# Kernel tuning notes

Hardware: AMD Instinct MI355X
Metric: run time of the kernel (lower is better)

The kernel has to match this reference:

```python
import jax, jax.numpy as jnp
import numpy as np

# xLSTM '80k' config: 4 blocks (mLSTM at 0,2,3; sLSTM at 1)
B, S, F = 128, 256, 10      # batch, seq (= context_length = forecast_horizon), features
E, NH = 40, 8               # d_model, heads
DH = E // NH                # 5,  sLSTM per-head dim
I = 128                     # mLSTM inner dim = round64(2*E)
QKB = 4; NQK = I // QKB     # q/k/v block-diagonal proj: 32 blocks of 4
MDH = I // NH               # 16, mLSTM per-head dim
FFD = 64                    # gated FFN dim = round64(1.3*E)
K = 4                       # causal conv kernel
NMB = 3                     # number of mLSTM blocks


def layer_norm(x, w, eps=1e-5):
    mu = x.mean(-1, keepdims=True)
    return (x - mu) * jax.lax.rsqrt(x.var(-1, keepdims=True) + eps) * w


def multihead_norm(x, w, nh, eps=1e-5):
    # per-head group norm over D//nh channels, weight only
    b, s, d = x.shape
    xh = x.reshape(b, s, nh, d // nh)
    xh = (xh - xh.mean(-1, keepdims=True)) * jax.lax.rsqrt(xh.var(-1, keepdims=True) + eps)
    return xh.reshape(b, s, d) * w


def causal_conv(x, w, b):
    # depthwise causal conv1d, kernel K; x: (B,S,C), w: (C,K)
    xt = x.transpose(0, 2, 1)
    y = jax.lax.conv_general_dilated(xt, w[:, None, :], (1,), [(K - 1, 0)],
                                     feature_group_count=x.shape[-1],
                                     dimension_numbers=('NCH', 'OIH', 'NCH'))
    return (y + b[None, :, None]).transpose(0, 2, 1)


def headwise(x, w):
    # block-diagonal linear (LinearHeadwiseExpand, no bias): w (nb, bo, bi)
    nb, bo, bi = w.shape
    xh = x.reshape(*x.shape[:-1], nb, bi)
    return jnp.einsum('bsni,noi->bsno', xh, w).reshape(*x.shape[:-1], nb * bo)


def pos_encoding():
    pos = jnp.arange(S, dtype=jnp.float32)[:, None]
    div = jnp.exp(jnp.arange(0, E, 2, dtype=jnp.float32) * (-np.log(10000.0) / E))
    pe = jnp.zeros((S, E), jnp.float32)
    pe = pe.at[:, 0::2].set(jnp.sin(pos * div))
    pe = pe.at[:, 1::2].set(jnp.cos(pos * div))
    return pe


def mlstm_layer(x, up_w, conv_w, conv_b, q_w, k_w, v_w, ig_w, ig_b, fg_w, fg_b, mhn_w, skip, down_w):
    x_m, z = jnp.split(x @ up_w.T, 2, axis=-1)                 # each (B,S,I)
    x_c = jax.nn.silu(causal_conv(x_m, conv_w, conv_b))
    q, k, v = headwise(x_c, q_w), headwise(x_c, k_w), headwise(x_m, v_w)
    gin = jnp.concatenate([q, k, v], axis=-1)                   # (B,S,3I)
    ip = (gin @ ig_w.T + ig_b).transpose(0, 2, 1)               # (B,NH,S)
    fp = (gin @ fg_w.T + fg_b).transpose(0, 2, 1)
    heads = lambda t: t.reshape(B, S, NH, MDH).transpose(0, 2, 1, 3)
    qh, kh, vh = heads(q), heads(k), heads(v)
    # stabilized parallel mLSTM (parallel_stabilized_simple)
    Fc = jnp.cumsum(jax.nn.log_sigmoid(fp), axis=-1)
    log_fg = Fc[..., :, None] - Fc[..., None, :]                # (B,NH,S,S)
    mask = jnp.tril(jnp.ones((S, S), bool))
    log_D = jnp.where(mask, log_fg, -jnp.inf) + ip[..., None, :]
    mD = jnp.max(log_D, axis=-1, keepdims=True)
    D = jnp.exp(log_D - mD)
    qk = jnp.einsum('bhsd,bhtd->bhst', qh, kh) * (MDH ** -0.5)
    C = qk * D
    nrm = jnp.maximum(jnp.abs(C.sum(-1, keepdims=True)), jnp.exp(-mD))
    h = jnp.einsum('bhst,bhtd->bhsd', C / (nrm + 1e-6), vh)
    h = multihead_norm(h.transpose(0, 2, 1, 3).reshape(B, S, I), mhn_w, NH)
    return ((h + skip * x_c) * jax.nn.silu(z)) @ down_w.T


def slstm_layer(x, conv_w, conv_b, wi, wf, wz, wo, R, bias, mhn_w):
    x_c = jax.nn.silu(causal_conv(x, conv_w, conv_b))
    g = lambda inp, w: headwise(inp, w).reshape(B, S, NH, DH)
    # i,f from conv path; z,o from raw input (order i,f,z,o)
    gx = jnp.stack([g(x_c, wi), g(x_c, wf), g(x, wz), g(x, wo)], axis=3)  # (B,S,NH,4,DH)
    gx = gx.transpose(1, 0, 2, 3, 4)                                      # (S,B,NH,4,DH)

    def step(carry, g_t):
        h, c, n, m = carry
        raw = g_t + jnp.einsum('bhd,hgde->bhge', h, R) + bias
        i_r, f_r, z_r, o_r = raw[:, :, 0], raw[:, :, 1], raw[:, :, 2], raw[:, :, 3]
        logfplusm = m + jax.nn.log_sigmoid(f_r)
        m_new = jnp.maximum(i_r, logfplusm)
        ig, fg = jnp.exp(i_r - m_new), jnp.exp(logfplusm - m_new)
        c_new = fg * c + ig * jnp.tanh(z_r)
        n_new = fg * n + ig
        h_new = jax.nn.sigmoid(o_r) * c_new / n_new
        return (h_new, c_new, n_new, m_new), h_new

    z0 = jnp.zeros((B, NH, DH), jnp.float32)
    _, hs = jax.lax.scan(step, (z0, z0, z0, z0), gx)
    return multihead_norm(hs.transpose(1, 0, 2, 3).reshape(B, S, E), mhn_w, NH)


def _forward(x, in_proj_w, in_proj_b, m_ln_w, m_up_w, m_conv_w, m_conv_b, m_q_w, m_k_w, m_v_w,
             m_ig_w, m_ig_b, m_fg_w, m_fg_b, m_mhn_w, m_skip, m_down_w,
             s_ln1_w, s_conv_w, s_conv_b, s_wi, s_wf, s_wz, s_wo, s_R, s_b, s_mhn_w,
             s_ln2_w, s_ff_up_w, s_ff_down_w, post_ln_w, out_w, out_b):
    h = x @ in_proj_w.T + in_proj_b + pos_encoding()
    mb = lambda h, j: h + mlstm_layer(layer_norm(h, m_ln_w[j]), m_up_w[j], m_conv_w[j], m_conv_b[j],
                                      m_q_w[j], m_k_w[j], m_v_w[j], m_ig_w[j], m_ig_b[j],
                                      m_fg_w[j], m_fg_b[j], m_mhn_w[j], m_skip[j], m_down_w[j])
    h = mb(h, 0)                       # block 0: mLSTM
    # block 1: sLSTM + gated FFN (pre-LN residual)
    h = h + slstm_layer(layer_norm(h, s_ln1_w), s_conv_w, s_conv_b, s_wi, s_wf, s_wz, s_wo, s_R, s_b, s_mhn_w)
    gpre, up = jnp.split(layer_norm(h, s_ln2_w) @ s_ff_up_w.T, 2, axis=-1)
    h = h + (jax.nn.gelu(gpre, approximate=False) * up) @ s_ff_down_w.T
    h = mb(h, 1)                       # block 2: mLSTM
    h = mb(h, 2)                       # block 3: mLSTM
    return layer_norm(h, post_ln_w) @ out_w.T + out_b


def setup_inputs():
    ks = iter(jax.random.split(jax.random.key(0), 64))
    rn = lambda shape, fan: jax.random.normal(next(ks), shape, jnp.float32) * (fan ** -0.5)
    d = {}
    d['x'] = jax.random.normal(next(ks), (B, S, F), jnp.float32)
    d['in_proj_w'] = rn((E, F), F); d['in_proj_b'] = jnp.zeros((E,), jnp.float32)
    d['m_ln_w'] = jnp.ones((NMB, E), jnp.float32)
    d['m_up_w'] = rn((NMB, 2 * I, E), E)
    d['m_conv_w'] = rn((NMB, I, K), K); d['m_conv_b'] = jnp.zeros((NMB, I), jnp.float32)
    d['m_q_w'] = rn((NMB, NQK, QKB, QKB), QKB)
    d['m_k_w'] = rn((NMB, NQK, QKB, QKB), QKB)
    d['m_v_w'] = rn((NMB, NQK, QKB, QKB), QKB)
    d['m_ig_w'] = rn((NMB, NH, 3 * I), 3 * I); d['m_ig_b'] = jnp.zeros((NMB, NH), jnp.float32)
    d['m_fg_w'] = rn((NMB, NH, 3 * I), 3 * I); d['m_fg_b'] = 3.0 * jnp.ones((NMB, NH), jnp.float32)
    d['m_mhn_w'] = jnp.ones((NMB, I), jnp.float32); d['m_skip'] = jnp.ones((NMB, I), jnp.float32)
    d['m_down_w'] = rn((NMB, E, I), I)
    d['s_ln1_w'] = jnp.ones((E,), jnp.float32)
    d['s_conv_w'] = rn((E, K), K); d['s_conv_b'] = jnp.zeros((E,), jnp.float32)
    d['s_wi'] = rn((NH, DH, DH), DH); d['s_wf'] = rn((NH, DH, DH), DH)
    d['s_wz'] = rn((NH, DH, DH), DH); d['s_wo'] = rn((NH, DH, DH), DH)
    d['s_R'] = rn((NH, 4, DH, DH), DH); d['s_b'] = jnp.zeros((NH, 4, DH), jnp.float32)
    d['s_mhn_w'] = jnp.ones((E,), jnp.float32); d['s_ln2_w'] = jnp.ones((E,), jnp.float32)
    d['s_ff_up_w'] = rn((2 * FFD, E), E); d['s_ff_down_w'] = rn((E, FFD), FFD)
    d['post_ln_w'] = jnp.ones((E,), jnp.float32)
    d['out_w'] = rn((1, E), E); d['out_b'] = jnp.zeros((1,), jnp.float32)
    return d


def reference(x, in_proj_w, in_proj_b, m_ln_w, m_up_w, m_conv_w, m_conv_b, m_q_w, m_k_w, m_v_w,
              m_ig_w, m_ig_b, m_fg_w, m_fg_b, m_mhn_w, m_skip, m_down_w,
              s_ln1_w, s_conv_w, s_conv_b, s_wi, s_wf, s_wz, s_wo, s_R, s_b, s_mhn_w,
              s_ln2_w, s_ff_up_w, s_ff_down_w, post_ln_w, out_w, out_b):
    return _forward(x, in_proj_w, in_proj_b, m_ln_w, m_up_w, m_conv_w, m_conv_b, m_q_w, m_k_w, m_v_w,
                    m_ig_w, m_ig_b, m_fg_w, m_fg_b, m_mhn_w, m_skip, m_down_w,
                    s_ln1_w, s_conv_w, s_conv_b, s_wi, s_wf, s_wz, s_wo, s_R, s_b, s_mhn_w,
                    s_ln2_w, s_ff_up_w, s_ff_down_w, post_ln_w, out_w, out_b)
```

## Files before the change

kernel.cpp:

```cpp
#include <hip/hip_runtime.h>
#include <math.h>

constexpr int cB = 128, cS = 256, cF = 10, cE = 40, cNH = 8, cDH = 5;
constexpr int cI = 128, cMDH = 16, cK = 4;

typedef __attribute__((ext_vector_type(8))) short short8v;
typedef __attribute__((ext_vector_type(4))) float f32x4;

#define BC8(v, l) __uint_as_float(__builtin_amdgcn_ds_swizzle(__float_as_uint(v), ((l) << 5) | 0x18))

__device__ __forceinline__ short f2bf(float f) {
    unsigned u = __float_as_uint(f);
    u += 0x7FFF + ((u >> 16) & 1);
    return (short)(u >> 16);
}

__global__ __launch_bounds__(256) void init_k(const float* __restrict__ x, const float* __restrict__ w,
                                              const float* __restrict__ b, float* __restrict__ h) {
    int idx = blockIdx.x * 256 + threadIdx.x;
    int e = idx % cE; int bs = idx / cE; int s = bs % cS;
    float acc = b[e];
    const float* xr = x + (size_t)bs * cF;
#pragma unroll
    for (int f = 0; f < cF; ++f) acc += xr[f] * w[e * cF + f];
    int i2 = e >> 1;
    float div = expf(-(float)(2 * i2) * (logf(10000.f) / 40.0f));
    float arg = (float)s * div;
    acc += (e & 1) ? cosf(arg) : sinf(arg);
    h[idx] = acc;
}

__global__ __launch_bounds__(256) void ln_up_k(const float* __restrict__ h, const float* __restrict__ lnw,
                                               const float* __restrict__ upw, float* __restrict__ xmz) {
    __shared__ float lnr[16][cE];
    __shared__ float wT[cE * 257];
    int row0 = blockIdx.x * 16;
    int tid = threadIdx.x;
    for (int j = tid; j < 2560; j += 256) {
        float4 v = ((const float4*)upw)[j];
        int o = j / 10, kq = (j - o * 10) * 4;
        wT[(kq + 0) * 257 + o] = v.x;
        wT[(kq + 1) * 257 + o] = v.y;
        wT[(kq + 2) * 257 + o] = v.z;
        wT[(kq + 3) * 257 + o] = v.w;
    }
    if (tid < 16) {
        const float* r = h + (size_t)(row0 + tid) * cE;
        float mu = 0.f;
        for (int k = 0; k < cE; ++k) mu += r[k];
        mu *= (1.f / cE);
        float va = 0.f;
        for (int k = 0; k < cE; ++k) { float d = r[k] - mu; va += d * d; }
        va *= (1.f / cE);
        float rs = rsqrtf(va + 1e-5f);
        for (int k = 0; k < cE; ++k) lnr[tid][k] = (r[k] - mu) * rs * lnw[k];
    }
    __syncthreads();
    int o = tid;
    float acc[16];
#pragma unroll
    for (int r = 0; r < 16; ++r) acc[r] = 0.f;
    for (int k = 0; k < cE; ++k) {
        float wv = wT[k * 257 + o];
#pragma unroll
        for (int r = 0; r < 16; ++r) acc[r] = fmaf(lnr[r][k], wv, acc[r]);
    }
#pragma unroll
    for (int r = 0; r < 16; ++r) xmz[(size_t)(row0 + r) * 256 + o] = acc[r];
}

template <int C>
__global__ __launch_bounds__(256) void conv_silu_k(const float* __restrict__ in, int instride,
                                                   const float* __restrict__ w, const float* __restrict__ bias,
                                                   float* __restrict__ out) {
    int idx = blockIdx.x * 256 + threadIdx.x;
    int c = idx % C; int bs = idx / C; int s = bs % cS;
    float acc = bias[c];
#pragma unroll
    for (int j = 0; j < cK; ++j) {
        int sj = s - 3 + j;
        if (sj >= 0) acc += in[(size_t)(bs + j - 3) * instride + c] * w[c * cK + j];
    }
    float sg = 1.f / (1.f + __expf(-acc));
    out[idx] = acc * sg;
}

__global__ __launch_bounds__(256) void qkv_k(const float* __restrict__ xc, const float* __restrict__ xmz,
                                             const float* __restrict__ qw, const float* __restrict__ kw,
                                             const float* __restrict__ vw,
                                             float* __restrict__ qb, float* __restrict__ kb, float* __restrict__ vb) {
    int idx = blockIdx.x * 256 + threadIdx.x;
    int c = idx & 127; int bs = idx >> 7;
    int n = c >> 2, o = c & 3;
    const float* xcr = xc + (size_t)bs * cI + n * 4;
    const float* xmr = xmz + (size_t)bs * 256 + n * 4;
    const float* qwp = qw + n * 16 + o * 4;
    const float* kwp = kw + n * 16 + o * 4;
    const float* vwp = vw + n * 16 + o * 4;
    float aq = 0, ak = 0, av = 0;
#pragma unroll
    for (int i = 0; i < 4; ++i) { float a = xcr[i], m = xmr[i]; aq += a * qwp[i]; ak += a * kwp[i]; av += m * vwp[i]; }
    qb[idx] = aq; kb[idx] = ak; vb[idx] = av;
}

__global__ __launch_bounds__(256, 2) void gates_k(const float* __restrict__ qb, const float* __restrict__ kb,
                                                  const float* __restrict__ vb, const float* __restrict__ igw,
                                                  const float* __restrict__ igb, const float* __restrict__ fgw,
                                                  const float* __restrict__ fgb,
                                                  float* __restrict__ ipb, float* __restrict__ fpb) {
    __shared__ float g[32 * 388];
    __shared__ float w[16 * 388];
    int row0 = blockIdx.x * 32;
    int tid = threadIdx.x;

    for (int i = tid; i < 16 * 96; i += 256) {
        int r = i / 96, c4 = i - r * 96;
        const float* src = (r < 8) ? (igw + r * 384) : (fgw + (r - 8) * 384);
        *(float4*)&w[r * 388 + c4 * 4] = ((const float4*)src)[c4];
    }
    for (int i = tid; i < 32 * 96; i += 256) {
        int r = i / 96, c4 = i - r * 96;
        size_t gr = (size_t)(row0 + r) * cI;
        const float4* src = (c4 < 32) ? (const float4*)(qb + gr) + c4
                          : (c4 < 64) ? (const float4*)(kb + gr) + (c4 - 32)
                                      : (const float4*)(vb + gr) + (c4 - 64);
        *(float4*)&g[r * 388 + c4 * 4] = *src;
    }
    __syncthreads();

    int rp = tid >> 3;
    int hp = tid & 7;
    int o0 = 2 * hp, o1 = o0 + 1;

    const float4* gp = (const float4*)(g + rp * 388);
    const float4* w0p = (const float4*)(w + o0 * 388);
    const float4* w1p = (const float4*)(w + o1 * 388);

    float a0e = 0.f, a0o = 0.f, a1e = 0.f, a1o = 0.f;
#pragma unroll 2
    for (int c4 = 0; c4 < 96; c4 += 2) {
        float4 gv0 = gp[c4], gv1 = gp[c4 + 1];
        float4 wa0 = w0p[c4], wa1 = w0p[c4 + 1];
        float4 wb0 = w1p[c4], wb1 = w1p[c4 + 1];
        a0e = fmaf(gv0.x, wa0.x, a0e); a0e = fmaf(gv0.y, wa0.y, a0e);
        a0e = fmaf(gv0.z, wa0.z, a0e); a0e = fmaf(gv0.w, wa0.w, a0e);
        a1e = fmaf(gv0.x, wb0.x, a1e); a1e = fmaf(gv0.y, wb0.y, a1e);
        a1e = fmaf(gv0.z, wb0.z, a1e); a1e = fmaf(gv0.w, wb0.w, a1e);
        a0o = fmaf(gv1.x, wa1.x, a0o); a0o = fmaf(gv1.y, wa1.y, a0o);
        a0o = fmaf(gv1.z, wa1.z, a0o); a0o = fmaf(gv1.w, wa1.w, a0o);
        a1o = fmaf(gv1.x, wb1.x, a1o); a1o = fmaf(gv1.y, wb1.y, a1o);
        a1o = fmaf(gv1.z, wb1.z, a1o); a1o = fmaf(gv1.w, wb1.w, a1o);
    }
    float a0 = a0e + a0o, a1 = a1e + a1o;

    int h0 = o0 & 7, wch0 = o0 >> 3;
    int h1 = o1 & 7, wch1 = o1 >> 3;
    float b0 = wch0 ? fgb[h0] : igb[h0];
    float b1 = wch1 ? fgb[h1] : igb[h1];
    int grow = row0 + rp;
    int bb = grow >> 8, ss = grow & 255;
    float* d0 = (wch0 ? fpb : ipb) + (size_t)(bb * cNH + h0) * cS + ss;
    float* d1 = (wch1 ? fpb : ipb) + (size_t)(bb * cNH + h1) * cS + ss;
    *d0 = a0 + b0; *d1 = a1 + b1;
}

constexpr int QKW = 24;
constexpr int VTW = 264;
constexpr int CBW = 280;

__global__ __launch_bounds__(256, 2) void attn_k(const float* __restrict__ qg, const float* __restrict__ kg,
                                                 const float* __restrict__ vg, const float* __restrict__ ipg,
                                                 const float* __restrict__ fpg, float* __restrict__ hatt) {
    int bh = blockIdx.x; int b = bh >> 3, h = bh & 7;
    int tid = threadIdx.x;
    int wid = tid >> 6, lane = tid & 63;
    int colL = lane & 15, grp = lane >> 4;

    __shared__ float sEA[cS], sMx[cS], sFc[cS];
    __shared__ short sQ[cS * QKW], sK[cS * QKW];
    __shared__ short sVt[cMDH * VTW];
    __shared__ short sC[4][16 * CBW];

    {
        const float4 fp4 = ((const float4*)(fpg + (size_t)bh * cS))[lane];
        const float4 ip4 = ((const float4*)(ipg + (size_t)bh * cS))[lane];
        float fpa[4] = {fp4.x, fp4.y, fp4.z, fp4.w};
        float ipa[4] = {ip4.x, ip4.y, ip4.z, ip4.w};
        float p[4];
        float run = 0.f;
#pragma unroll
        for (int i = 0; i < 4; ++i) {
            float xx = fpa[i];
            float lsg = fminf(xx, 0.f) - log1pf(expf(-fabsf(xx)));
            run += lsg; p[i] = run;
        }
        float cum = p[3];
#pragma unroll
        for (int off = 1; off < 64; off <<= 1) { float t = __shfl_up(cum, off); if (lane >= off) cum += t; }
        float excl = cum - p[3];
        float aa[4];
#pragma unroll
        for (int i = 0; i < 4; ++i) {
            float fcv = excl + p[i];
            aa[i] = ipa[i] - fcv;
            sFc[lane * 4 + i] = fcv;
            sEA[lane * 4 + i] = __expf(aa[i]);
        }
        float mq[4]; mq[0] = aa[0];
#pragma unroll
        for (int i = 1; i < 4; ++i) mq[i] = fmaxf(mq[i - 1], aa[i]);
        float cm = mq[3];
#pragma unroll
        for (int off = 1; off < 64; off <<= 1) { float t = __shfl_up(cm, off); if (lane >= off) cm = fmaxf(cm, t); }
        float exm = __shfl_up(cm, 1);
        if (lane == 0) exm = -3.0e38f;
#pragma unroll
        for (int i = 0; i < 4; ++i) sMx[lane * 4 + i] = fmaxf(exm, mq[i]);
    }

    {
        int t = tid;
        const float4* qp = (const float4*)(qg + ((size_t)(b * cS) + t) * cI + h * cMDH);
        const float4* kp = (const float4*)(kg + ((size_t)(b * cS) + t) * cI + h * cMDH);
        const float4* vp = (const float4*)(vg + ((size_t)(b * cS) + t) * cI + h * cMDH);
        float4 q0 = qp[0], q1 = qp[1], q2 = qp[2], q3 = qp[3];
        float4 k0 = kp[0], k1 = kp[1], k2 = kp[2], k3 = kp[3];
        float4 v0 = vp[0], v1 = vp[1], v2 = vp[2], v3 = vp[3];
        short8v qa, qbv, ka, kbv;
        qa[0] = f2bf(q0.x); qa[1] = f2bf(q0.y); qa[2] = f2bf(q0.z); qa[3] = f2bf(q0.w);
        qa[4] = f2bf(q1.x); qa[5] = f2bf(q1.y); qa[6] = f2bf(q1.z); qa[7] = f2bf(q1.w);
        qbv[0] = f2bf(q2.x); qbv[1] = f2bf(q2.y); qbv[2] = f2bf(q2.z); qbv[3] = f2bf(q2.w);
        qbv[4] = f2bf(q3.x); qbv[5] = f2bf(q3.y); qbv[6] = f2bf(q3.z); qbv[7] = f2bf(q3.w);
        ka[0] = f2bf(k0.x); ka[1] = f2bf(k0.y); ka[2] = f2bf(k0.z); ka[3] = f2bf(k0.w);
        ka[4] = f2bf(k1.x); ka[5] = f2bf(k1.y); ka[6] = f2bf(k1.z); ka[7] = f2bf(k1.w);
        kbv[0] = f2bf(k2.x); kbv[1] = f2bf(k2.y); kbv[2] = f2bf(k2.z); kbv[3] = f2bf(k2.w);
        kbv[4] = f2bf(k3.x); kbv[5] = f2bf(k3.y); kbv[6] = f2bf(k3.z); kbv[7] = f2bf(k3.w);
        *(short8v*)(sQ + t * QKW) = qa;
        *(short8v*)(sQ + t * QKW + 8) = qbv;
        *(short8v*)(sK + t * QKW) = ka;
        *(short8v*)(sK + t * QKW + 8) = kbv;
        sVt[0 * VTW + t] = f2bf(v0.x);  sVt[1 * VTW + t] = f2bf(v0.y);
        sVt[2 * VTW + t] = f2bf(v0.z);  sVt[3 * VTW + t] = f2bf(v0.w);
        sVt[4 * VTW + t] = f2bf(v1.x);  sVt[5 * VTW + t] = f2bf(v1.y);
        sVt[6 * VTW + t] = f2bf(v1.z);  sVt[7 * VTW + t] = f2bf(v1.w);
        sVt[8 * VTW + t] = f2bf(v2.x);  sVt[9 * VTW + t] = f2bf(v2.y);
        sVt[10 * VTW + t] = f2bf(v2.z); sVt[11 * VTW + t] = f2bf(v2.w);
        sVt[12 * VTW + t] = f2bf(v3.x); sVt[13 * VTW + t] = f2bf(v3.y);
        sVt[14 * VTW + t] = f2bf(v3.z); sVt[15 * VTW + t] = f2bf(v3.w);
    }
    __syncthreads();

    const short one_bf = (short)0x3F80;
    short8v ones = {one_bf, one_bf, one_bf, one_bf, one_bf, one_bf, one_bf, one_bf};
    short8v kz = {0, 0, 0, 0, 0, 0, 0, 0};
    short* Cb = sC[wid];
    const int tiles[4] = {wid, 7 - wid, 8 + wid, 15 - wid};

    for (int sti = 0; sti < 4; ++sti) {
        int st = tiles[sti];
        int s0 = st * 16;

        float eMx4[4], flr4[4];
#pragma unroll
        for (int j = 0; j < 4; ++j) {
            int sg = s0 + grp * 4 + j;
            eMx4[j] = 0.25f * __expf(-sMx[sg]);
            flr4[j] = __expf(-(sFc[sg] + sMx[sg]));
        }

        if ((st & 1) == 0) {
#pragma unroll
            for (int z = 0; z < 4; ++z) {
                int idx = lane * 4 + z;
                Cb[(idx >> 4) * CBW + (st + 1) * 16 + (idx & 15)] = 0;
            }
        }

        short8v aQ = (grp < 2) ? *(const short8v*)(sQ + (s0 + colL) * QKW + grp * 8) : kz;

        for (int tt = 0; tt <= st; ++tt) {
            int t0 = tt * 16;
            short8v bK = (grp < 2) ? *(const short8v*)(sK + (t0 + colL) * QKW + grp * 8) : kz;
            f32x4 zacc = {0.f, 0.f, 0.f, 0.f};
            f32x4 d = __builtin_amdgcn_mfma_f32_16x16x32_bf16(aQ, bK, zacc, 0, 0, 0);
            float ea = sEA[t0 + colL];
#pragma unroll
            for (int j = 0; j < 4; ++j) {
                float v = d[j] * (ea * eMx4[j]);
                if (tt == st) v = (colL <= grp * 4 + j) ? v : 0.f;
                Cb[(grp * 4 + j) * CBW + t0 + colL] = f2bf(v);
            }
        }

        f32x4 hacc = {0.f, 0.f, 0.f, 0.f};
        f32x4 sacc = {0.f, 0.f, 0.f, 0.f};
        int nch = (st + 2) >> 1;
        for (int c = 0; c < nch; ++c) {
            int tc = c * 32;
            short8v aC = *(const short8v*)(Cb + colL * CBW + tc + grp * 8);
            short8v bV = *(const short8v*)(sVt + colL * VTW + tc + grp * 8);
            hacc = __builtin_amdgcn_mfma_f32_16x16x32_bf16(aC, bV, hacc, 0, 0, 0);
            sacc = __builtin_amdgcn_mfma_f32_16x16x32_bf16(aC, ones, sacc, 0, 0, 0);
        }

#pragma unroll
        for (int j = 0; j < 4; ++j) {
            int sg = s0 + grp * 4 + j;
            float nrm = fmaxf(fabsf(sacc[j]), flr4[j]) + 1e-6f;
            hatt[((size_t)(b * cS) + sg) * cI + h * cMDH + colL] = hacc[j] / nrm;
        }
    }
}

__global__ __launch_bounds__(320) void down_mhn_k(const float* __restrict__ hatt, const float* __restrict__ xc,
                                                  const float* __restrict__ xmz, const float* __restrict__ mhnw,
                                                  const float* __restrict__ skip, const float* __restrict__ dw,
                                                  float* __restrict__ h) {
    __shared__ float yl[8 * 128];
    int row0 = blockIdx.x * 8;
    int tid = threadIdx.x;
    for (int i = tid; i < 1024; i += 320) yl[i] = hatt[(size_t)row0 * cI + i];
    __syncthreads();
    if (tid < 64) {
        int r = tid >> 3, hh = tid & 7;
        int row = row0 + r;
        float* g = yl + r * 128 + hh * 16;
        float xv[16];
        float mu = 0.f;
#pragma unroll
        for (int d = 0; d < 16; ++d) { xv[d] = g[d]; mu += xv[d]; }
        mu *= (1.f / 16);
        float va = 0.f;
#pragma unroll
        for (int d = 0; d < 16; ++d) { float dd = xv[d] - mu; va += dd * dd; }
        va *= (1.f / 16);
        float rs = rsqrtf(va + 1e-5f);
        const float* xcr = xc + (size_t)row * cI + hh * 16;
        const float* zr  = xmz + (size_t)row * 256 + 128 + hh * 16;
#pragma unroll
        for (int d = 0; d < 16; ++d) {
            int i = hh * 16 + d;
            float z = zr[d];
            float sg = 1.f / (1.f + __expf(-z));
            g[d] = ((xv[d] - mu) * rs * mhnw[i] + skip[i] * xcr[d]) * (z * sg);
        }
    }
    __syncthreads();
    int r = tid / 40, e = tid % 40;
    const float* dr = dw + e * cI;
    const float* yr = yl + r * cI;
    float acc = 0.f;
    for (int i = 0; i < cI; ++i) acc += yr[i] * dr[i];
    h[(size_t)(row0 + r) * cE + e] += acc;
}

__global__ __launch_bounds__(256) void ln_rows_k(const float* __restrict__ h, const float* __restrict__ w,
                                                 float* __restrict__ out) {
    int rid = blockIdx.x * 256 + threadIdx.x;
    const float* r = h + (size_t)rid * cE;
    float mu = 0;
    for (int k = 0; k < cE; ++k) mu += r[k];
    mu *= (1.f / cE);
    float va = 0;
    for (int k = 0; k < cE; ++k) { float d = r[k] - mu; va += d * d; }
    va *= (1.f / cE);
    float rs = rsqrtf(va + 1e-5f);
    float* o = out + (size_t)rid * cE;
    for (int k = 0; k < cE; ++k) o[k] = (r[k] - mu) * rs * w[k];
}

__global__ __launch_bounds__(256) void sgates_k(const float* __restrict__ xcs, const float* __restrict__ ln1,
                                                const float* __restrict__ wi, const float* __restrict__ wf,
                                                const float* __restrict__ wz, const float* __restrict__ wo,
                                                float* __restrict__ gall) {
    int idx = blockIdx.x * 256 + threadIdx.x;
    int g = idx & 3; int r1 = idx >> 2;
    int e = r1 % 5; int r2 = r1 / 5;
    int bh = r2 & 1023; int s = r2 >> 10;
    int b = bh >> 3, h = bh & 7;
    const float* in = (g < 2) ? xcs : ln1;
    const float* w = (g == 0) ? wi : (g == 1) ? wf : (g == 2) ? wz : wo;
    const float* ir = in + ((size_t)(b * cS) + s) * cE + h * cDH;
    const float* wp = w + h * 25 + e * 5;
    float acc = 0.f;
#pragma unroll
    for (int i = 0; i < 5; ++i) acc += ir[i] * wp[i];
    gall[idx] = acc;
}

__global__ __launch_bounds__(64) void scan_k(const float* __restrict__ gall, const float* __restrict__ R,
                                             const float* __restrict__ bias, const float* __restrict__ mhnw,
                                             float* __restrict__ hbuf) {
    int lane = threadIdx.x;
    int grp = lane >> 3;
    int e = lane & 7;
    int ee = e < 5 ? e : 4;
    int bh = blockIdx.x * 8 + grp;
    int h = bh & 7;

    __shared__ float sOut[8][1285];

    float Rr[4][5];
#pragma unroll
    for (int g = 0; g < 4; ++g)
#pragma unroll
        for (int d = 0; d < 5; ++d) Rr[g][d] = R[h * 100 + g * 25 + d * 5 + ee];
    float bg[4];
#pragma unroll
    for (int g = 0; g < 4; ++g) bg[g] = bias[h * 20 + g * 5 + ee];
    float wmh = mhnw[h * 5 + ee];

    const float4* gp = (const float4*)gall + ((size_t)bh * 5 + ee);

    float4 rg[16];
#pragma unroll
    for (int j = 0; j < 16; ++j) rg[j] = gp[(size_t)j * 5120];

    float cstate = 0.f, nstate = 0.f, mstate = 0.f;
    float hs0 = 0.f, hs1 = 0.f, hs2 = 0.f, hs3 = 0.f, hs4 = 0.f;

    for (int t = 0; t < cS; t += 16) {
#pragma unroll
        for (int j = 0; j < 16; ++j) {
            float4 g4 = rg[j];
            rg[j] = gp[(size_t)(t + j + 16) * 5120];

            float ir = g4.x + bg[0], fr = g4.y + bg[1], zr = g4.z + bg[2], orr = g4.w + bg[3];
            ir = fmaf(hs0, Rr[0][0], ir); fr = fmaf(hs0, Rr[1][0], fr);
            zr = fmaf(hs0, Rr[2][0], zr); orr = fmaf(hs0, Rr[3][0], orr);
            ir = fmaf(hs1, Rr[0][1], ir); fr = fmaf(hs1, Rr[1][1], fr);
            zr = fmaf(hs1, Rr[2][1], zr); orr = fmaf(hs1, Rr[3][1], orr);
            ir = fmaf(hs2, Rr[0][2], ir); fr = fmaf(hs2, Rr[1][2], fr);
            zr = fmaf(hs2, Rr[2][2], zr); orr = fmaf(hs2, Rr[3][2], orr);
            ir = fmaf(hs3, Rr[0][3], ir); fr = fmaf(hs3, Rr[1][3], fr);
            zr = fmaf(hs3, Rr[2][3], zr); orr = fmaf(hs3, Rr[3][3], orr);
            ir = fmaf(hs4, Rr[0][4], ir); fr = fmaf(hs4, Rr[1][4], fr);
            zr = fmaf(hs4, Rr[2][4], zr); orr = fmaf(hs4, Rr[3][4], orr);

            float lsg = fminf(fr, 0.f) - __logf(1.f + __expf(-fabsf(fr)));
            float lfm = mstate + lsg;
            float mn = fmaxf(ir, lfm);
            float ig = __expf(ir - mn), fg = __expf(lfm - mn);
            float th = 1.f - 2.f * __builtin_amdgcn_rcpf(__expf(2.f * zr) + 1.f);
            float cn = fg * cstate + ig * th;
            float nn = fg * nstate + ig;
            float sg = __builtin_amdgcn_rcpf(1.f + __expf(-orr));
            float hn = sg * cn * __builtin_amdgcn_rcpf(nn);
            cstate = cn; nstate = nn; mstate = mn;

            hs0 = BC8(hn, 0); hs1 = BC8(hn, 1); hs2 = BC8(hn, 2);
            hs3 = BC8(hn, 3); hs4 = BC8(hn, 4);
            float mu = ((hs0 + hs1) + (hs2 + hs3) + hs4) * 0.2f;
            float d0 = hs0 - mu, d1 = hs1 - mu, d2 = hs2 - mu, d3 = hs3 - mu, d4 = hs4 - mu;
            float va = (d0 * d0 + d1 * d1 + d2 * d2 + d3 * d3 + d4 * d4) * 0.2f;
            float rs = __builtin_amdgcn_rsqf(va + 1e-5f);
            if (e < 5) sOut[grp][(t + j) * 5 + e] = (hn - mu) * rs * wmh;
        }
    }
    __syncthreads();

    for (int i = lane; i < 8 * 1280; i += 64) {
        int c = i / 1280;
        int r = i - c * 1280;
        int tt = r / 5, e2 = r - tt * 5;
        int bh2 = blockIdx.x * 8 + c;
        int b2 = bh2 >> 3, h2 = bh2 & 7;
        float* hp = hbuf + ((size_t)b2 * cS + tt) * cE + h2 * cDH + e2;
        *hp += sOut[c][r];
    }
}

__global__ __launch_bounds__(256) void ff_k(float* __restrict__ h, const float* __restrict__ lnw,
                                            const float* __restrict__ upw, const float* __restrict__ dnw) {
    __shared__ float lnr[8][cE];
    __shared__ float ffr[8][64];
    int row0 = blockIdx.x * 8;
    int tid = threadIdx.x;
    if (tid < 8) {
        const float* r = h + (size_t)(row0 + tid) * cE;
        float mu = 0;
        for (int k = 0; k < cE; ++k) mu += r[k];
        mu *= (1.f / cE);
        float va = 0;
        for (int k = 0; k < cE; ++k) { float d = r[k] - mu; va += d * d; }
        va *= (1.f / cE);
        float rs = rsqrtf(va + 1e-5f);
        for (int k = 0; k < cE; ++k) lnr[tid][k] = (r[k] - mu) * rs * lnw[k];
    }
    __syncthreads();
    {
        int r = tid >> 5;
        int f0 = (tid & 31) * 2;
#pragma unroll
        for (int ff = 0; ff < 2; ++ff) {
            int f = f0 + ff;
            float a = 0, u = 0;
            const float* wa = upw + f * cE;
            const float* wu = upw + (64 + f) * cE;
            for (int k = 0; k < cE; ++k) {
                float xv = lnr[r][k];
                a = fmaf(xv, wa[k], a);
                u = fmaf(xv, wu[k], u);
            }
            float g = 0.5f * a * (1.f + erff(a * 0.70710678118f));
            ffr[r][f] = g * u;
        }
    }
    __syncthreads();
    for (int i = tid; i < 320; i += 256) {
        int r = i / 40, e = i - r * 40;
        const float* dr = dnw + e * 64;
        const float* fr = ffr[r];
        float acc = 0.f;
        for (int k = 0; k < 64; ++k) acc = fmaf(fr[k], dr[k], acc);
        h[(size_t)(row0 + r) * cE + e] += acc;
    }
}

__global__ __launch_bounds__(256) void final_k(const float* __restrict__ h, const float* __restrict__ lnw,
                                               const float* __restrict__ ow, const float* __restrict__ ob,
                                               float* __restrict__ out) {
    int rid = blockIdx.x * 256 + threadIdx.x;
    const float* r = h + (size_t)rid * cE;
    float mu = 0;
    for (int k = 0; k < cE; ++k) mu += r[k];
    mu *= (1.f / cE);
    float va = 0;
    for (int k = 0; k < cE; ++k) { float d = r[k] - mu; va += d * d; }
    va *= (1.f / cE);
    float rs = rsqrtf(va + 1e-5f);
    float acc = ob[0];
    for (int k = 0; k < cE; ++k) acc += (r[k] - mu) * rs * lnw[k] * ow[k];
    out[rid] = acc;
}

extern "C" void kernel_launch(void* const* d_in, const int* in_sizes, int n_in,
                              void* d_out, int out_size, void* d_ws, size_t ws_size,
                              hipStream_t stream) {
    const float* x        = (const float*)d_in[0];
    const float* in_w     = (const float*)d_in[1];
    const float* in_b     = (const float*)d_in[2];
    const float* m_ln_w   = (const float*)d_in[3];
    const float* m_up_w   = (const float*)d_in[4];
    const float* m_conv_w = (const float*)d_in[5];
    const float* m_conv_b = (const float*)d_in[6];
    const float* m_q_w    = (const float*)d_in[7];
    const float* m_k_w    = (const float*)d_in[8];
    const float* m_v_w    = (const float*)d_in[9];
    const float* m_ig_w   = (const float*)d_in[10];
    const float* m_ig_b   = (const float*)d_in[11];
    const float* m_fg_w   = (const float*)d_in[12];
    const float* m_fg_b   = (const float*)d_in[13];
    const float* m_mhn_w  = (const float*)d_in[14];
    const float* m_skip   = (const float*)d_in[15];
    const float* m_down_w = (const float*)d_in[16];
    const float* s_ln1_w  = (const float*)d_in[17];
    const float* s_conv_w = (const float*)d_in[18];
    const float* s_conv_b = (const float*)d_in[19];
    const float* s_wi     = (const float*)d_in[20];
    const float* s_wf     = (const float*)d_in[21];
    const float* s_wz     = (const float*)d_in[22];
    const float* s_wo     = (const float*)d_in[23];
    const float* s_R      = (const float*)d_in[24];
    const float* s_bias   = (const float*)d_in[25];
    const float* s_mhn_w  = (const float*)d_in[26];
    const float* s_ln2_w  = (const float*)d_in[27];
    const float* s_ff_up  = (const float*)d_in[28];
    const float* s_ff_dn  = (const float*)d_in[29];
    const float* post_ln_w= (const float*)d_in[30];
    const float* out_w    = (const float*)d_in[31];
    const float* out_b    = (const float*)d_in[32];

    float* ws   = (float*)d_ws;
    float* h    = ws;
    float* xmz  = h + 1310720;
    float* xc   = xmz + 8388608;
    float* qb   = xc + 4194304;
    float* kb   = qb + 4194304;
    float* vb   = kb + 4194304;
    float* ipb  = vb + 4194304;
    float* fpb  = ipb + 262144;
    float* hatt = fpb + 262144;
    float* lnbuf = xmz;
    float* xcs   = xmz + 1310720;
    float* gall  = xmz + 2621440;

    init_k<<<5120, 256, 0, stream>>>(x, in_w, in_b, h);

    auto mlstm = [&](int j) {
        ln_up_k<<<2048, 256, 0, stream>>>(h, m_ln_w + j * cE, m_up_w + (size_t)j * 256 * cE, xmz);
        conv_silu_k<128><<<16384, 256, 0, stream>>>(xmz, 256, m_conv_w + j * cI * cK, m_conv_b + j * cI, xc);
        qkv_k<<<16384, 256, 0, stream>>>(xc, xmz, m_q_w + j * 512, m_k_w + j * 512, m_v_w + j * 512, qb, kb, vb);
        gates_k<<<1024, 256, 0, stream>>>(qb, kb, vb, m_ig_w + j * cNH * 384, m_ig_b + j * cNH,
                                          m_fg_w + j * cNH * 384, m_fg_b + j * cNH, ipb, fpb);
        attn_k<<<1024, 256, 0, stream>>>(qb, kb, vb, ipb, fpb, hatt);
        down_mhn_k<<<4096, 320, 0, stream>>>(hatt, xc, xmz, m_mhn_w + j * cI, m_skip + j * cI,
                                             m_down_w + j * cE * cI, h);
    };

    mlstm(0);

    ln_rows_k<<<128, 256, 0, stream>>>(h, s_ln1_w, lnbuf);
    conv_silu_k<40><<<5120, 256, 0, stream>>>(lnbuf, 40, s_conv_w, s_conv_b, xcs);
    sgates_k<<<20480, 256, 0, stream>>>(xcs, lnbuf, s_wi, s_wf, s_wz, s_wo, gall);
    scan_k<<<128, 64, 0, stream>>>(gall, s_R, s_bias, s_mhn_w, h);

    ff_k<<<4096, 256, 0, stream>>>(h, s_ln2_w, s_ff_up, s_ff_dn);

    mlstm(1);
    mlstm(2);

    final_k<<<128, 256, 0, stream>>>(h, post_ln_w, out_w, out_b, (float*)d_out);
}
```

Measured before the change: 851.9 us.

## Restructure mLSTM attention to 32x32 MFMA tiles with streaming C·V accumulation

The attention kernel moves from 16x16 query/key tiles to 32x32x16 MFMA tiles, so the head dim of 16 fills the K dimension instead of zero-padding half the lanes. The C·V product is accumulated per key chunk inside the key loop, so the full score row buffer shrinks from 16x280 to 32x40 per wave. Row sums now come from fp32 adds plus a shuffle reduction instead of a second MFMA against ones. exp(-M) and the floor term are precomputed once per position during setup. Together these cut LDS use enough to raise the occupancy hint from 2 to 3 blocks per CU. The risk is extra LDS write/read hazards within a wave on the small C buffer, since there is no explicit barrier between writing and reading it, and more register pressure from the 16-element arrays.

```diff
diff --git a/kernel.cpp b/kernel.cpp
--- a/kernel.cpp
+++ b/kernel.cpp
@@ -6,6 +6,7 @@
 
 typedef __attribute__((ext_vector_type(8))) short short8v;
 typedef __attribute__((ext_vector_type(4))) float f32x4;
+typedef __attribute__((ext_vector_type(16))) float f32x16;
 
 #define BC8(v, l) __uint_as_float(__builtin_amdgcn_ds_swizzle(__float_as_uint(v), ((l) << 5) | 0x18))
 
@@ -166,20 +167,22 @@
 
 constexpr int QKW = 24;
 constexpr int VTW = 264;
-constexpr int CBW = 280;
-
-__global__ __launch_bounds__(256, 2) void attn_k(const float* __restrict__ qg, const float* __restrict__ kg,
+constexpr int CBW = 40;
+
+__global__ __launch_bounds__(256, 3) void attn_k(const float* __restrict__ qg, const float* __restrict__ kg,
                                                  const float* __restrict__ vg, const float* __restrict__ ipg,
                                                  const float* __restrict__ fpg, float* __restrict__ hatt) {
     int bh = blockIdx.x; int b = bh >> 3, h = bh & 7;
     int tid = threadIdx.x;
     int wid = tid >> 6, lane = tid & 63;
     int colL = lane & 15, grp = lane >> 4;
-
-    __shared__ float sEA[cS], sMx[cS], sFc[cS];
+    int col32 = lane & 31, hi = lane >> 5;
+
+    __shared__ float sEA[cS], sEMx[cS], sFlr[cS];
     __shared__ short sQ[cS * QKW], sK[cS * QKW];
     __shared__ short sVt[cMDH * VTW];
-    __shared__ short sC[4][16 * CBW];
+    __shared__ short sCb[4][32 * CBW];
+    __shared__ float sSum[4][32];
 
     {
         const float4 fp4 = ((const float4*)(fpg + (size_t)bh * cS))[lane];
@@ -198,12 +201,11 @@
 #pragma unroll
         for (int off = 1; off < 64; off <<= 1) { float t = __shfl_up(cum, off); if (lane >= off) cum += t; }
         float excl = cum - p[3];
-        float aa[4];
+        float aa[4], fcv4[4];
 #pragma unroll
         for (int i = 0; i < 4; ++i) {
-            float fcv = excl + p[i];
-            aa[i] = ipa[i] - fcv;
-            sFc[lane * 4 + i] = fcv;
+            fcv4[i] = excl + p[i];
+            aa[i] = ipa[i] - fcv4[i];
             sEA[lane * 4 + i] = __expf(aa[i]);
         }
         float mq[4]; mq[0] = aa[0];
@@ -215,7 +217,11 @@
         float exm = __shfl_up(cm, 1);
         if (lane == 0) exm = -3.0e38f;
 #pragma unroll
-        for (int i = 0; i < 4; ++i) sMx[lane * 4 + i] = fmaxf(exm, mq[i]);
+        for (int i = 0; i < 4; ++i) {
+            float Mx = fmaxf(exm, mq[i]);
+            sEMx[lane * 4 + i] = 0.25f * __expf(-Mx);
+            sFlr[lane * 4 + i] = __expf(-(fcv4[i] + Mx));
+        }
     }
 
     {
@@ -250,64 +256,72 @@
     }
     __syncthreads();
 
-    const short one_bf = (short)0x3F80;
-    short8v ones = {one_bf, one_bf, one_bf, one_bf, one_bf, one_bf, one_bf, one_bf};
-    short8v kz = {0, 0, 0, 0, 0, 0, 0, 0};
-    short* Cb = sC[wid];
-    const int tiles[4] = {wid, 7 - wid, 8 + wid, 15 - wid};
-
-    for (int sti = 0; sti < 4; ++sti) {
-        int st = tiles[sti];
-        int s0 = st * 16;
-
-        float eMx4[4], flr4[4];
-#pragma unroll
-        for (int j = 0; j < 4; ++j) {
-            int sg = s0 + grp * 4 + j;
-            eMx4[j] = 0.25f * __expf(-sMx[sg]);
-            flr4[j] = __expf(-(sFc[sg] + sMx[sg]));
-        }
-
-        if ((st & 1) == 0) {
-#pragma unroll
-            for (int z = 0; z < 4; ++z) {
-                int idx = lane * 4 + z;
-                Cb[(idx >> 4) * CBW + (st + 1) * 16 + (idx & 15)] = 0;
+    short* Cb = sCb[wid];
+    float* Sm = sSum[wid];
+    const int tiles2[2] = {wid, 7 - wid};
+
+    for (int sti = 0; sti < 2; ++sti) {
+        int st = tiles2[sti];
+        int s0 = st * 32;
+
+        short8v aQ = *(const short8v*)(sQ + (s0 + col32) * QKW + hi * 8);
+        int r16[16]; float eMx16[16];
+#pragma unroll
+        for (int reg = 0; reg < 16; ++reg) {
+            int r = (reg & 3) + 8 * (reg >> 2) + 4 * hi;
+            r16[reg] = r;
+            eMx16[reg] = sEMx[s0 + r];
+        }
+        float sum16[16];
+#pragma unroll
+        for (int reg = 0; reg < 16; ++reg) sum16[reg] = 0.f;
+        f32x4 hacc0 = {0.f, 0.f, 0.f, 0.f}, hacc1 = {0.f, 0.f, 0.f, 0.f};
+
+        for (int tt = 0; tt <= st; ++tt) {
+            int t0 = tt * 32;
+            short8v bK = *(const short8v*)(sK + (t0 + col32) * QKW + hi * 8);
+            f32x16 zz = {0.f, 0.f, 0.f, 0.f, 0.f, 0.f, 0.f, 0.f,
+                         0.f, 0.f, 0.f, 0.f, 0.f, 0.f, 0.f, 0.f};
+            f32x16 d = __builtin_amdgcn_mfma_f32_32x32x16_bf16(aQ, bK, zz, 0, 0, 0);
+            float ea = sEA[t0 + col32];
+            bool diag = (tt == st);
+#pragma unroll
+            for (int reg = 0; reg < 16; ++reg) {
+                float v = d[reg] * (ea * eMx16[reg]);
+                if (diag && col32 > r16[reg]) v = 0.f;
+                sum16[reg] += v;
+                Cb[r16[reg] * CBW + col32] = f2bf(v);
             }
-        }
-
-        short8v aQ = (grp < 2) ? *(const short8v*)(sQ + (s0 + colL) * QKW + grp * 8) : kz;
-
-        for (int tt = 0; tt <= st; ++tt) {
-            int t0 = tt * 16;
-            short8v bK = (grp < 2) ? *(const short8v*)(sK + (t0 + colL) * QKW + grp * 8) : kz;
-            f32x4 zacc = {0.f, 0.f, 0.f, 0.f};
-            f32x4 d = __builtin_amdgcn_mfma_f32_16x16x32_bf16(aQ, bK, zacc, 0, 0, 0);
-            float ea = sEA[t0 + colL];
+            short8v bV  = *(const short8v*)(sVt + colL * VTW + t0 + grp * 8);
+            short8v aC0 = *(const short8v*)(Cb + colL * CBW + grp * 8);
+            hacc0 = __builtin_amdgcn_mfma_f32_16x16x32_bf16(aC0, bV, hacc0, 0, 0, 0);
+            short8v aC1 = *(const short8v*)(Cb + (16 + colL) * CBW + grp * 8);
+            hacc1 = __builtin_amdgcn_mfma_f32_16x16x32_bf16(aC1, bV, hacc1, 0, 0, 0);
+        }
+
+#pragma unroll
+        for (int reg = 0; reg < 16; ++reg) {
+            float s = sum16[reg];
+#pragma unroll
+            for (int m = 1; m < 32; m <<= 1) s += __shfl_xor(s, m);
+            sum16[reg] = s;
+        }
+        if (col32 == 0) {
+#pragma unroll
+            for (int reg = 0; reg < 16; ++reg) Sm[r16[reg]] = sum16[reg];
+        }
+
+#pragma unroll
+        for (int sub = 0; sub < 2; ++sub) {
+            f32x4 hacc = sub ? hacc1 : hacc0;
 #pragma unroll
             for (int j = 0; j < 4; ++j) {
-                float v = d[j] * (ea * eMx4[j]);
-                if (tt == st) v = (colL <= grp * 4 + j) ? v : 0.f;
-                Cb[(grp * 4 + j) * CBW + t0 + colL] = f2bf(v);
+                int rloc = sub * 16 + grp * 4 + j;
+                int sr = s0 + rloc;
+                float sC = Sm[rloc];
+                float nrm = fmaxf(fabsf(sC), sFlr[sr]) + 1e-6f;
+                hatt[((size_t)(b * cS) + sr) * cI + h * cMDH + colL] = hacc[j] / nrm;
             }
-        }
-
-        f32x4 hacc = {0.f, 0.f, 0.f, 0.f};
-        f32x4 sacc = {0.f, 0.f, 0.f, 0.f};
-        int nch = (st + 2) >> 1;
-        for (int c = 0; c < nch; ++c) {
-            int tc = c * 32;
-            short8v aC = *(const short8v*)(Cb + colL * CBW + tc + grp * 8);
-            short8v bV = *(const short8v*)(sVt + colL * VTW + tc + grp * 8);
-            hacc = __builtin_amdgcn_mfma_f32_16x16x32_bf16(aC, bV, hacc, 0, 0, 0);
-            sacc = __builtin_amdgcn_mfma_f32_16x16x32_bf16(aC, ones, sacc, 0, 0, 0);
-        }
-
-#pragma unroll
-        for (int j = 0; j < 4; ++j) {
-            int sg = s0 + grp * 4 + j;
-            float nrm = fmaxf(fabsf(sacc[j]), flr4[j]) + 1e-6f;
-            hatt[((size_t)(b * cS) + sg) * cI + h * cMDH + colL] = hacc[j] / nrm;
         }
     }
 }
```

Result: no change. 841.2 us (-1.3%).
